# Optimization experiments

Measured on AMD Instinct MI355X. Metric: run time of the kernel, lower is better.

Reference implementation:

```python
import jax, jax.numpy as jnp
import numpy as np

D_MODEL = 128
NHEAD = 8
NLAYERS = 6
LAYER_NAMES = ['self', 'cross', 'self', 'cross', 'self', 'cross']
TEMPERATURE = 5.0
EPS = 1e-6


def _pos_encoding(x):
    # Sinusoidal 1D position encoding along the width axis. x: [N, H, W, C]
    C, W = x.shape[-1], x.shape[2]
    pos = jnp.arange(W, dtype=x.dtype)[:, None]                      # [W,1]
    div = jnp.exp(jnp.arange(0, C, 2, dtype=x.dtype) * (-np.log(10000.0) / C))
    pe = jnp.zeros((W, C), x.dtype)
    pe = pe.at[:, 0::2].set(jnp.sin(pos * div))
    pe = pe.at[:, 1::2].set(jnp.cos(pos * div))
    return x + pe[None, None]                                        # broadcast over N,H


def _linear_attention(q, k, v):
    # q,k,v: [N, H, W, nhead, dim]; kernelized linear attention along W
    Q = jax.nn.elu(q) + 1.0
    K = jax.nn.elu(k) + 1.0
    v_len = v.shape[2]
    V = v / v_len
    KV = jnp.einsum('nhsed,nhsev->nhedv', K, V)                      # [N,H,e,d,d]
    Z = 1.0 / (jnp.einsum('nhled,nhed->nhle', Q, K.sum(axis=2)) + EPS)
    return jnp.einsum('nhled,nhedv,nhle->nhlev', Q, KV, Z) * v_len


def _layer_norm(x, g, b):
    m = x.mean(-1, keepdims=True)
    v = jnp.mean((x - m) ** 2, -1, keepdims=True)
    return (x - m) / jnp.sqrt(v + 1e-5) * g + b


def _encoder_layer(x, source, Wq, Wk, Wv, Wm, W1, W2, g1, b1, g2, b2):
    x = _pos_encoding(x)
    source = _pos_encoding(source)
    bs, h, w, c = x.shape
    e, d = NHEAD, c // NHEAD
    q = (x @ Wq).reshape(bs, h, w, e, d)
    k = (source @ Wk).reshape(bs, h, w, e, d)
    v = (source @ Wv).reshape(bs, h, w, e, d)
    msg = _linear_attention(q, k, v).reshape(bs, h, w, c) @ Wm
    msg = _layer_norm(msg, g1, b1)
    msg = jnp.concatenate([x, msg], axis=-1)                         # [N,H,W,2C]
    msg = jax.nn.relu(msg @ W1) @ W2
    msg = _layer_norm(msg, g2, b2)
    return x + msg


def _forward(feat0, feat1, Wq, Wk, Wv, Wm, W1, W2, g1, b1, g2, b2):
    feat0 = feat0.transpose(0, 2, 3, 1)                              # [N,H,W,C]
    feat1 = feat1.transpose(0, 2, 3, 1)
    for i, name in enumerate(LAYER_NAMES):
        p = (Wq[i], Wk[i], Wv[i], Wm[i], W1[i], W2[i], g1[i], b1[i], g2[i], b2[i])
        if name == 'self':
            feat0 = _encoder_layer(feat0, feat0, *p)
            feat1 = _encoder_layer(feat1, feat1, *p)
        else:  # cross: sequential update (feat1 sees updated feat0), as in torch source
            feat0 = _encoder_layer(feat0, feat1, *p)
            feat1 = _encoder_layer(feat1, feat0, *p)
    w = feat0.shape[2]
    attn_mask = jnp.where(jnp.triu(jnp.ones((w, w), bool), 1), -jnp.inf, 0.0)
    attn_mask = attn_mask[None, None].astype(feat0.dtype)
    scale = feat0.shape[-1] ** 0.5
    sim = jnp.einsum('ntwc,ntlc->ntwl', feat0 / scale, feat1 / scale) / TEMPERATURE
    return sim + attn_mask


def setup_inputs() -> dict:
    key = jax.random.key(0)
    ks = jax.random.split(key, 12)
    N, C, H, W = 2, D_MODEL, 64, 640
    L, D = NLAYERS, D_MODEL
    s = 1.0 / np.sqrt(D)
    s2 = 1.0 / np.sqrt(2 * D)
    return {
        'feat0': jax.random.normal(ks[0], (N, C, H, W), jnp.float32),
        'feat1': jax.random.normal(ks[1], (N, C, H, W), jnp.float32),
        'Wq': jax.random.normal(ks[2], (L, D, D), jnp.float32) * s,
        'Wk': jax.random.normal(ks[3], (L, D, D), jnp.float32) * s,
        'Wv': jax.random.normal(ks[4], (L, D, D), jnp.float32) * s,
        'Wm': jax.random.normal(ks[5], (L, D, D), jnp.float32) * s,
        'W1': jax.random.normal(ks[6], (L, 2 * D, 2 * D), jnp.float32) * s2,
        'W2': jax.random.normal(ks[7], (L, 2 * D, D), jnp.float32) * s2,
        'g1': jnp.ones((L, D), jnp.float32),
        'b1': jnp.zeros((L, D), jnp.float32),
        'g2': jnp.ones((L, D), jnp.float32),
        'b2': jnp.zeros((L, D), jnp.float32),
    }


def reference(feat0, feat1, Wq, Wk, Wv, Wm, W1, W2, g1, b1, g2, b2):
    return _forward(feat0, feat1, Wq, Wk, Wv, Wm, W1, W2, g1, b1, g2, b2)
```

## Files before the change

### kernel.cpp

```cpp
#include <hip/hip_runtime.h>
#include <cmath>
#include <math.h>

#define TOK 81920
#define WDIM 640

typedef __attribute__((ext_vector_type(8))) short short8v;
typedef __attribute__((ext_vector_type(4))) float f32x4;

__device__ __forceinline__ short f2bf(float f) {
  union { float f; unsigned u; } x; x.f = f;
  unsigned r = (x.u + 0x7fffu + ((x.u >> 16) & 1u)) >> 16;
  return (short)r;
}
__device__ __forceinline__ float bf2f(short s) {
  union { unsigned u; float f; } x; x.u = ((unsigned)(unsigned short)s) << 16;
  return x.f;
}

__global__ __launch_bounds__(256) void pe_kernel(float* __restrict__ pe) {
  int id = blockIdx.x * 256 + threadIdx.x;
  if (id >= WDIM * 128) return;
  int w = id >> 7;
  int c = id & 127;
  float i2 = (float)(c & 126);
  float freq = expf(i2 * -0.071955784156063941f);
  float ang = (float)w * freq;
  pe[id] = (c & 1) ? cosf(ang) : sinf(ang);
}

__global__ __launch_bounds__(256) void tr_kernel(const float* __restrict__ in0,
                                                 const float* __restrict__ in1,
                                                 short* __restrict__ x0,
                                                 short* __restrict__ x1) {
  __shared__ float t[32][33];
  int w0 = blockIdx.x * 32;
  int c0 = blockIdx.y * 32;
  int z = blockIdx.z;
  int feat = z >> 7;
  int nh = z & 127;
  int n = nh >> 6, h = nh & 63;
  const float* in = feat ? in1 : in0;
  short* out = feat ? x1 : x0;
  int tx = threadIdx.x & 31, ty = threadIdx.x >> 5;
  const float* ip = in + ((n * 128 + c0) * 64 + h) * 640 + w0;
#pragma unroll
  for (int i = 0; i < 32; i += 8)
    t[ty + i][tx] = ip[(ty + i) * (64 * 640) + tx];
  __syncthreads();
  short* op = out + ((size_t)(n * 64 + h) * 640 + w0) * 128 + c0;
#pragma unroll
  for (int i = 0; i < 32; i += 8)
    op[(size_t)(ty + i) * 128 + tx] = f2bf(t[tx][ty + i]);
}

__global__ __launch_bounds__(256) void wprep_kernel(
    const float* __restrict__ Wq, const float* __restrict__ Wk,
    const float* __restrict__ Wv, const float* __restrict__ Wm,
    const float* __restrict__ W1, const float* __restrict__ W2,
    short* __restrict__ BT) {
  int id = blockIdx.x * 256 + threadIdx.x;
  if (id >= 6 * 163840) return;
  int layer = id / 163840;
  int r = id % 163840;
  float v;
  if (r < 65536) {
    int seg = r >> 14;
    int rr = r & 16383;
    int n = rr >> 7, k = rr & 127;
    const float* W = seg == 0 ? Wq : seg == 1 ? Wk : seg == 2 ? Wv : Wm;
    v = W[layer * 16384 + k * 128 + n];
  } else if (r < 131072) {
    int rr = r - 65536;
    int n = rr >> 8, k = rr & 255;
    v = W1[layer * 65536 + k * 256 + n];
  } else {
    int rr = r - 131072;
    int n = rr >> 8, k = rr & 255;
    v = W2[layer * 32768 + k * 128 + n];
  }
  BT[id] = f2bf(v);
}

__device__ __forceinline__ void load_af(const short* __restrict__ A,
                                        const float* __restrict__ pe,
                                        int bm, int wr, int l15, int lk,
                                        short8v af[4][4]) {
  const int wbase = bm % WDIM;
#pragma unroll
  for (int mf = 0; mf < 4; ++mf) {
    const int rl = wr * 64 + mf * 16 + l15;
    const short* ar = A + (size_t)(bm + rl) * 128;
    const float* pr = pe + (size_t)(wbase + rl) * 128;
#pragma unroll
    for (int ks = 0; ks < 4; ++ks) {
      const int kloc = ks * 32 + lk * 8;
      short8v xa = *(const short8v*)(ar + kloc);
      f32x4 p0 = *(const f32x4*)(pr + kloc);
      f32x4 p1 = *(const f32x4*)(pr + kloc + 4);
      short8v o;
      o[0] = f2bf(bf2f(xa[0]) + p0[0]); o[1] = f2bf(bf2f(xa[1]) + p0[1]);
      o[2] = f2bf(bf2f(xa[2]) + p0[2]); o[3] = f2bf(bf2f(xa[3]) + p0[3]);
      o[4] = f2bf(bf2f(xa[4]) + p1[0]); o[5] = f2bf(bf2f(xa[5]) + p1[1]);
      o[6] = f2bf(bf2f(xa[6]) + p1[2]); o[7] = f2bf(bf2f(xa[7]) + p1[3]);
      af[ks][mf] = o;
    }
  }
}

__device__ __forceinline__ void proj_pass(const short8v af[4][4],
                                          const short* __restrict__ WT,
                                          int bm, int wr, int wc, int l15, int lk,
                                          short* __restrict__ out) {
  f32x4 acc[4][4] = {};
#pragma unroll
  for (int ks = 0; ks < 4; ++ks) {
    const int kloc = ks * 32 + lk * 8;
    short8v bfr[4];
#pragma unroll
    for (int nf = 0; nf < 4; ++nf)
      bfr[nf] = *(const short8v*)&WT[(size_t)(wc * 64 + nf * 16 + l15) * 128 + kloc];
#pragma unroll
    for (int mf = 0; mf < 4; ++mf)
#pragma unroll
      for (int nf = 0; nf < 4; ++nf)
        acc[mf][nf] = __builtin_amdgcn_mfma_f32_16x16x32_bf16(
            af[ks][mf], bfr[nf], acc[mf][nf], 0, 0, 0);
  }
#pragma unroll
  for (int mf = 0; mf < 4; ++mf)
#pragma unroll
    for (int nf = 0; nf < 4; ++nf) {
      const int colL = wc * 64 + nf * 16 + l15;
#pragma unroll
      for (int r = 0; r < 4; ++r) {
        const int row = bm + wr * 64 + mf * 16 + lk * 4 + r;
        out[(size_t)row * 128 + colL] = f2bf(acc[mf][nf][r]);
      }
    }
}

__global__ __launch_bounds__(256) void qkv_self_kernel(
    const short* __restrict__ x0, const short* __restrict__ x1,
    const float* __restrict__ pe,
    const short* __restrict__ wqT, const short* __restrict__ wkT,
    const short* __restrict__ wvT,
    short* q0, short* k0, short* v0, short* q1, short* k1, short* v1) {
  const int tid = threadIdx.x, lane = tid & 63, wid = tid >> 6;
  const int wr = wid >> 1, wc = wid & 1;
  const int bm = blockIdx.x * 128;
  const int l15 = lane & 15, lk = lane >> 4;
  const int z = blockIdx.z;
  const short* A = z ? x1 : x0;
  short8v af[4][4];
  load_af(A, pe, bm, wr, l15, lk, af);
  proj_pass(af, wqT, bm, wr, wc, l15, lk, z ? q1 : q0);
  proj_pass(af, wkT, bm, wr, wc, l15, lk, z ? k1 : k0);
  proj_pass(af, wvT, bm, wr, wc, l15, lk, z ? v1 : v0);
}

__global__ __launch_bounds__(256) void qkv_cross_kernel(
    const short* __restrict__ xq, const short* __restrict__ xs,
    const float* __restrict__ pe,
    const short* __restrict__ wqT, const short* __restrict__ wkT,
    const short* __restrict__ wvT,
    short* qb, short* kb, short* vb) {
  const int tid = threadIdx.x, lane = tid & 63, wid = tid >> 6;
  const int wr = wid >> 1, wc = wid & 1;
  const int bm = blockIdx.x * 128;
  const int l15 = lane & 15, lk = lane >> 4;
  short8v af[4][4];
  if (blockIdx.y == 0) {
    load_af(xq, pe, bm, wr, l15, lk, af);
    proj_pass(af, wqT, bm, wr, wc, l15, lk, qb);
  } else {
    load_af(xs, pe, bm, wr, l15, lk, af);
    proj_pass(af, wkT, bm, wr, wc, l15, lk, kb);
    proj_pass(af, wvT, bm, wr, wc, l15, lk, vb);
  }
}

template <int NSC>
__global__ __launch_bounds__(256) void kv_kernel(
    const short* __restrict__ k0, const short* __restrict__ v0,
    const short* __restrict__ k1, const short* __restrict__ v1,
    float* __restrict__ kvp) {
  const int bid = blockIdx.x;
  const int sc = bid % NSC;
  const int e = bid / NSC;
  const int strip = sc / 5, chunk = sc % 5;
  const short* kb = (strip >= 128) ? k1 : k0;
  const short* vb = (strip >= 128) ? v1 : v0;
  const int nh = strip & 127;
  const size_t base = (size_t)nh * (640 * 128) + (size_t)chunk * (128 * 128) + e * 16;
  __shared__ float Ks[128][16];
  __shared__ float Vs[128][16];
  const int tid = threadIdx.x;
  const int srow = tid >> 1, shalf = (tid & 1) * 8;
  short8v k8 = *(const short8v*)&kb[base + (size_t)srow * 128 + shalf];
  short8v v8 = *(const short8v*)&vb[base + (size_t)srow * 128 + shalf];
#pragma unroll
  for (int j = 0; j < 8; ++j) {
    float kr = bf2f(k8[j]);
    Ks[srow][shalf + j] = kr > 0.f ? kr + 1.f : __expf(kr);
    Vs[srow][shalf + j] = bf2f(v8[j]);
  }
  __syncthreads();
  const int d = tid >> 4, vv = tid & 15;
  float kv = 0.f, ks = 0.f;
#pragma unroll 8
  for (int sl = 0; sl < 128; ++sl) {
    float kk = Ks[sl][d];
    kv = fmaf(kk, Vs[sl][vv], kv);
    ks += kk;
  }
  float* out = kvp + ((size_t)(strip * 8 + e) * 5 + chunk) * 272;
  out[d * 16 + vv] = kv;
  if (vv == 0) out[256 + d] = ks;
}

template <int DUAL>
__global__ __launch_bounds__(256) void apply_kernel(
    short* q0, short* q1, const float* __restrict__ kvp) {
  const int bid = blockIdx.x;
  const int strip = bid / 10, lc = bid % 10;
  __shared__ float KV8[8][16][17];
  __shared__ float KS8[8][16];
  const int tid = threadIdx.x;
  for (int idx = tid; idx < 8 * 272; idx += 256) {
    int e = idx / 272, r = idx - e * 272;
    const float* p = kvp + ((size_t)(strip * 8 + e) * 5) * 272 + r;
    float s = ((p[0] + p[272]) + (p[544] + p[816])) + p[1088];
    if (r < 256) KV8[e][r >> 4][r & 15] = s;
    else         KS8[e][r - 256] = s;
  }
  __syncthreads();
  short* qb = (DUAL && strip >= 128) ? q1 : q0;
  const int nh = strip & 127;
  const int row = lc * 64 + (tid >> 2);
  const int cb = (tid & 3) * 32;
  short* qp = qb + (size_t)nh * (640 * 128) + (size_t)row * 128 + cb;
  short8v qv0 = *(const short8v*)(qp);
  short8v qv1 = *(const short8v*)(qp + 8);
  short8v qv2 = *(const short8v*)(qp + 16);
  short8v qv3 = *(const short8v*)(qp + 24);
  float qe[32];
#pragma unroll
  for (int j = 0; j < 8; ++j) {
    float a = bf2f(qv0[j]); qe[j]      = a > 0.f ? a + 1.f : __expf(a);
    float b = bf2f(qv1[j]); qe[8 + j]  = b > 0.f ? b + 1.f : __expf(b);
    float c = bf2f(qv2[j]); qe[16 + j] = c > 0.f ? c + 1.f : __expf(c);
    float d = bf2f(qv3[j]); qe[24 + j] = d > 0.f ? d + 1.f : __expf(d);
  }
  short res[32];
#pragma unroll
  for (int h = 0; h < 2; ++h) {
    const int e = (cb >> 4) + h;
    const float* Q = qe + h * 16;
    float dz = 0.f;
#pragma unroll
    for (int dd = 0; dd < 16; ++dd) dz = fmaf(Q[dd], KS8[e][dd], dz);
    const float zi = 1.f / (dz + 1e-6f);
#pragma unroll
    for (int vv = 0; vv < 16; ++vv) {
      float o = 0.f;
#pragma unroll
      for (int dd = 0; dd < 16; ++dd) o = fmaf(Q[dd], KV8[e][dd][vv], o);
      res[h * 16 + vv] = f2bf(o * zi);
    }
  }
  short8v w0, w1, w2, w3;
#pragma unroll
  for (int j = 0; j < 8; ++j) {
    w0[j] = res[j]; w1[j] = res[8 + j]; w2[j] = res[16 + j]; w3[j] = res[24 + j];
  }
  *(short8v*)(qp)      = w0;
  *(short8v*)(qp + 8)  = w1;
  *(short8v*)(qp + 16) = w2;
  *(short8v*)(qp + 24) = w3;
}

__global__ __launch_bounds__(256) void wm_ln_kernel(
    short* oA, short* oB, const short* __restrict__ wmT,
    const float* __restrict__ g, const float* __restrict__ b) {
  const int z = blockIdx.z;
  short* o = z ? oB : oA;
  __shared__ float lds_s[2][128];
  __shared__ float lds_q[2][128];
  const int tid = threadIdx.x, lane = tid & 63, wid = tid >> 6;
  const int wr = wid >> 1, wc = wid & 1;
  const int bm = blockIdx.x * 128;
  const int l15 = lane & 15, lk = lane >> 4;
  f32x4 acc[4][4] = {};
#pragma unroll
  for (int ks = 0; ks < 4; ++ks) {
    const int kloc = ks * 32 + lk * 8;
    short8v bfr[4], afr[4];
#pragma unroll
    for (int nf = 0; nf < 4; ++nf)
      bfr[nf] = *(const short8v*)&wmT[(size_t)(wc * 64 + nf * 16 + l15) * 128 + kloc];
#pragma unroll
    for (int mf = 0; mf < 4; ++mf)
      afr[mf] = *(const short8v*)&o[(size_t)(bm + wr * 64 + mf * 16 + l15) * 128 + kloc];
#pragma unroll
    for (int mf = 0; mf < 4; ++mf)
#pragma unroll
      for (int nf = 0; nf < 4; ++nf)
        acc[mf][nf] = __builtin_amdgcn_mfma_f32_16x16x32_bf16(
            afr[mf], bfr[nf], acc[mf][nf], 0, 0, 0);
  }
#pragma unroll
  for (int mf = 0; mf < 4; ++mf)
#pragma unroll
    for (int r = 0; r < 4; ++r) {
      float s = acc[mf][0][r] + acc[mf][1][r] + acc[mf][2][r] + acc[mf][3][r];
      float qq = acc[mf][0][r] * acc[mf][0][r] + acc[mf][1][r] * acc[mf][1][r]
               + acc[mf][2][r] * acc[mf][2][r] + acc[mf][3][r] * acc[mf][3][r];
#pragma unroll
      for (int off = 1; off < 16; off <<= 1) {
        s += __shfl_xor(s, off);
        qq += __shfl_xor(qq, off);
      }
      if (l15 == 0) {
        int rl = wr * 64 + mf * 16 + lk * 4 + r;
        lds_s[wc][rl] = s;
        lds_q[wc][rl] = qq;
      }
    }
  __syncthreads();
  float gv[4], bv[4];
#pragma unroll
  for (int nf = 0; nf < 4; ++nf) {
    int c = wc * 64 + nf * 16 + l15;
    gv[nf] = g[c]; bv[nf] = b[c];
  }
#pragma unroll
  for (int mf = 0; mf < 4; ++mf)
#pragma unroll
    for (int r = 0; r < 4; ++r) {
      int rl = wr * 64 + mf * 16 + lk * 4 + r;
      float mean = (lds_s[0][rl] + lds_s[1][rl]) * (1.f / 128.f);
      float var = (lds_q[0][rl] + lds_q[1][rl]) * (1.f / 128.f) - mean * mean;
      float rstd = rsqrtf(var + 1e-5f);
#pragma unroll
      for (int nf = 0; nf < 4; ++nf) {
        float val = (acc[mf][nf][r] - mean) * rstd * gv[nf] + bv[nf];
        o[(size_t)(bm + rl) * 128 + wc * 64 + nf * 16 + l15] = f2bf(val);
      }
    }
}

__global__ __launch_bounds__(256) void w1_kernel(
    const short* __restrict__ xA, const short* __restrict__ xB,
    const short* __restrict__ mA, const short* __restrict__ mB,
    const float* __restrict__ pe, const short* __restrict__ w1T,
    short* h0A, short* h1A, short* h0B, short* h1B) {
  const int z = blockIdx.z;
  const short* x = z ? xB : xA;
  const short* m = z ? mB : mA;
  short* h0 = z ? h0B : h0A;
  short* h1 = z ? h1B : h1A;
  const int tid = threadIdx.x, lane = tid & 63, wid = tid >> 6;
  const int wr = wid >> 1, wc = wid & 1;
  const int bm = blockIdx.x * 128;
  const int l15 = lane & 15, lk = lane >> 4;
  const int wbase = bm % WDIM;
  for (int p = 0; p < 2; ++p) {
    f32x4 acc[4][4] = {};
#pragma unroll
    for (int ks = 0; ks < 8; ++ks) {
      const int kloc = ks * 32 + lk * 8;
      short8v bfr[4], afr[4];
#pragma unroll
      for (int nf = 0; nf < 4; ++nf)
        bfr[nf] = *(const short8v*)&w1T[(size_t)(p * 128 + wc * 64 + nf * 16 + l15) * 256 + kloc];
      if (ks < 4) {
#pragma unroll
        for (int mf = 0; mf < 4; ++mf) {
          const int rl = wr * 64 + mf * 16 + l15;
          short8v xa = *(const short8v*)(x + (size_t)(bm + rl) * 128 + kloc);
          const float* pr = pe + (size_t)(wbase + rl) * 128 + kloc;
          f32x4 p0 = *(const f32x4*)pr;
          f32x4 p1 = *(const f32x4*)(pr + 4);
          short8v ov;
          ov[0] = f2bf(bf2f(xa[0]) + p0[0]); ov[1] = f2bf(bf2f(xa[1]) + p0[1]);
          ov[2] = f2bf(bf2f(xa[2]) + p0[2]); ov[3] = f2bf(bf2f(xa[3]) + p0[3]);
          ov[4] = f2bf(bf2f(xa[4]) + p1[0]); ov[5] = f2bf(bf2f(xa[5]) + p1[1]);
          ov[6] = f2bf(bf2f(xa[6]) + p1[2]); ov[7] = f2bf(bf2f(xa[7]) + p1[3]);
          afr[mf] = ov;
        }
      } else {
#pragma unroll
        for (int mf = 0; mf < 4; ++mf)
          afr[mf] = *(const short8v*)&m[(size_t)(bm + wr * 64 + mf * 16 + l15) * 128 + kloc - 128];
      }
#pragma unroll
      for (int mf = 0; mf < 4; ++mf)
#pragma unroll
        for (int nf = 0; nf < 4; ++nf)
          acc[mf][nf] = __builtin_amdgcn_mfma_f32_16x16x32_bf16(
              afr[mf], bfr[nf], acc[mf][nf], 0, 0, 0);
    }
    short* h = p ? h1 : h0;
#pragma unroll
    for (int mf = 0; mf < 4; ++mf)
#pragma unroll
      for (int nf = 0; nf < 4; ++nf) {
        const int colL = wc * 64 + nf * 16 + l15;
#pragma unroll
        for (int r = 0; r < 4; ++r) {
          const int row = bm + wr * 64 + mf * 16 + lk * 4 + r;
          h[(size_t)row * 128 + colL] = f2bf(fmaxf(acc[mf][nf][r], 0.f));
        }
      }
  }
}

__global__ __launch_bounds__(256) void w2_ln_kernel(
    const short* __restrict__ h0A, const short* __restrict__ h1A,
    const short* __restrict__ h0B, const short* __restrict__ h1B,
    const short* __restrict__ w2T, short* xA, short* xB,
    const float* __restrict__ pe, const float* __restrict__ g,
    const float* __restrict__ b) {
  const int z = blockIdx.z;
  const short* h0 = z ? h0B : h0A;
  const short* h1 = z ? h1B : h1A;
  short* x = z ? xB : xA;
  __shared__ float lds_s[2][128];
  __shared__ float lds_q[2][128];
  const int tid = threadIdx.x, lane = tid & 63, wid = tid >> 6;
  const int wr = wid >> 1, wc = wid & 1;
  const int bm = blockIdx.x * 128;
  const int l15 = lane & 15, lk = lane >> 4;
  const int wbase = bm % WDIM;
  f32x4 acc[4][4] = {};
#pragma unroll
  for (int ks = 0; ks < 8; ++ks) {
    const int kloc = ks * 32 + lk * 8;
    const short* hp = (ks < 4) ? h0 : h1;
    const int kl = (ks < 4) ? kloc : kloc - 128;
    short8v bfr[4], afr[4];
#pragma unroll
    for (int nf = 0; nf < 4; ++nf)
      bfr[nf] = *(const short8v*)&w2T[(size_t)(wc * 64 + nf * 16 + l15) * 256 + kloc];
#pragma unroll
    for (int mf = 0; mf < 4; ++mf)
      afr[mf] = *(const short8v*)&hp[(size_t)(bm + wr * 64 + mf * 16 + l15) * 128 + kl];
#pragma unroll
    for (int mf = 0; mf < 4; ++mf)
#pragma unroll
      for (int nf = 0; nf < 4; ++nf)
        acc[mf][nf] = __builtin_amdgcn_mfma_f32_16x16x32_bf16(
            afr[mf], bfr[nf], acc[mf][nf], 0, 0, 0);
  }
#pragma unroll
  for (int mf = 0; mf < 4; ++mf)
#pragma unroll
    for (int r = 0; r < 4; ++r) {
      float s = acc[mf][0][r] + acc[mf][1][r] + acc[mf][2][r] + acc[mf][3][r];
      float qq = acc[mf][0][r] * acc[mf][0][r] + acc[mf][1][r] * acc[mf][1][r]
               + acc[mf][2][r] * acc[mf][2][r] + acc[mf][3][r] * acc[mf][3][r];
#pragma unroll
      for (int off = 1; off < 16; off <<= 1) {
        s += __shfl_xor(s, off);
        qq += __shfl_xor(qq, off);
      }
      if (l15 == 0) {
        int rl = wr * 64 + mf * 16 + lk * 4 + r;
        lds_s[wc][rl] = s;
        lds_q[wc][rl] = qq;
      }
    }
  __syncthreads();
  float gv[4], bv[4];
#pragma unroll
  for (int nf = 0; nf < 4; ++nf) {
    int c = wc * 64 + nf * 16 + l15;
    gv[nf] = g[c]; bv[nf] = b[c];
  }
#pragma unroll
  for (int mf = 0; mf < 4; ++mf)
#pragma unroll
    for (int r = 0; r < 4; ++r) {
      int rl = wr * 64 + mf * 16 + lk * 4 + r;
      float mean = (lds_s[0][rl] + lds_s[1][rl]) * (1.f / 128.f);
      float var = (lds_q[0][rl] + lds_q[1][rl]) * (1.f / 128.f) - mean * mean;
      float rstd = rsqrtf(var + 1e-5f);
      int row = bm + rl;
#pragma unroll
      for (int nf = 0; nf < 4; ++nf) {
        int col = wc * 64 + nf * 16 + l15;
        float ln = (acc[mf][nf][r] - mean) * rstd * gv[nf] + bv[nf];
        size_t xi = (size_t)row * 128 + col;
        float xv = bf2f(x[xi]) + pe[(size_t)(wbase + rl) * 128 + col] + ln;
        x[xi] = f2bf(xv);
      }
    }
}

__global__ __launch_bounds__(256) void sim_mfma(const short* __restrict__ f0,
                                                const short* __restrict__ f1,
                                                float* __restrict__ out) {
  const int fid = (blockIdx.z * 5 + blockIdx.y) * 5 + blockIdx.x;
  const int c8 = fid & 7, kk_ = fid >> 3;
  const int nt = c8 * 16 + kk_ / 25;
  const int r2 = kk_ % 25;
  const int bw = (r2 % 5) * 128;
  const int bl = (r2 / 5) * 128;
  const int tid = threadIdx.x;
  const int lane = tid & 63;
  const int wid = tid >> 6;
  const int wr = wid >> 1, wc = wid & 1;
  const short* __restrict__ A = f0 + (size_t)nt * 640 * 128;
  const short* __restrict__ B = f1 + (size_t)nt * 640 * 128;
  const int l15 = lane & 15;
  const int lk = lane >> 4;
  f32x4 acc[4][4] = {};
#pragma unroll
  for (int ks = 0; ks < 4; ++ks) {
    const int kloc = ks * 32 + lk * 8;
    short8v afr[4], bfr[4];
#pragma unroll
    for (int mf = 0; mf < 4; ++mf)
      afr[mf] = *(const short8v*)&A[(size_t)(bw + wr * 64 + mf * 16 + l15) * 128 + kloc];
#pragma unroll
    for (int nf = 0; nf < 4; ++nf)
      bfr[nf] = *(const short8v*)&B[(size_t)(bl + wc * 64 + nf * 16 + l15) * 128 + kloc];
#pragma unroll
    for (int mf = 0; mf < 4; ++mf)
#pragma unroll
      for (int nf = 0; nf < 4; ++nf)
        acc[mf][nf] = __builtin_amdgcn_mfma_f32_16x16x32_bf16(
            afr[mf], bfr[nf], acc[mf][nf], 0, 0, 0);
  }
#pragma unroll
  for (int mf = 0; mf < 4; ++mf)
#pragma unroll
    for (int nf = 0; nf < 4; ++nf) {
      const int l = bl + wc * 64 + nf * 16 + l15;
#pragma unroll
      for (int r = 0; r < 4; ++r) {
        const int w = bw + wr * 64 + mf * 16 + lk * 4 + r;
        float v = acc[mf][nf][r] * (1.f / 640.f);
        if (l > w) v = -1e30f;
        out[((size_t)nt * 640 + w) * 640 + l] = v;
      }
    }
}

extern "C" void kernel_launch(void* const* d_in, const int* in_sizes, int n_in,
                              void* d_out, int out_size, void* d_ws, size_t ws_size,
                              hipStream_t stream) {
  (void)in_sizes; (void)n_in; (void)out_size; (void)ws_size;
  const float* feat0 = (const float*)d_in[0];
  const float* feat1 = (const float*)d_in[1];
  const float* Wq = (const float*)d_in[2];
  const float* Wk = (const float*)d_in[3];
  const float* Wv = (const float*)d_in[4];
  const float* Wm = (const float*)d_in[5];
  const float* W1 = (const float*)d_in[6];
  const float* W2 = (const float*)d_in[7];
  const float* g1 = (const float*)d_in[8];
  const float* b1 = (const float*)d_in[9];
  const float* g2 = (const float*)d_in[10];
  const float* b2 = (const float*)d_in[11];

  float* wsf = (float*)d_ws;
  const size_t U = (size_t)TOK * 128;
  float* pe = wsf;
  short* x0 = (short*)(wsf + 81920);
  short* x1 = x0 + U;
  short* q0 = x1 + U;
  short* k0 = q0 + U;
  short* v0 = k0 + U;
  short* q1 = v0 + U;
  short* k1 = q1 + U;
  short* v1 = k1 + U;
  short* bt = v1 + U;
  float* kvp = (float*)(bt + 983040);

  dim3 blk(256);
  pe_kernel<<<dim3(320), blk, 0, stream>>>(pe);
  tr_kernel<<<dim3(20, 4, 256), blk, 0, stream>>>(feat0, feat1, x0, x1);
  wprep_kernel<<<dim3((6 * 163840 + 255) / 256), blk, 0, stream>>>(
      Wq, Wk, Wv, Wm, W1, W2, bt);

  const int NB = TOK / 128;
  for (int i = 0; i < 6; ++i) {
    const short* bt_i = bt + (size_t)i * 163840;
    const short* wqT = bt_i;
    const short* wkT = bt_i + 16384;
    const short* wvT = bt_i + 32768;
    const short* wmT = bt_i + 49152;
    const short* w1T = bt_i + 65536;
    const short* w2T = bt_i + 131072;
    const float* g1_i = g1 + i * 128;
    const float* b1_i = b1 + i * 128;
    const float* g2_i = g2 + i * 128;
    const float* b2_i = b2 + i * 128;
    if ((i & 1) == 0) {
      qkv_self_kernel<<<dim3(NB, 1, 2), blk, 0, stream>>>(
          x0, x1, pe, wqT, wkT, wvT, q0, k0, v0, q1, k1, v1);
      kv_kernel<1280><<<dim3(8 * 1280), blk, 0, stream>>>(k0, v0, k1, v1, kvp);
      apply_kernel<1><<<dim3(2560), blk, 0, stream>>>(q0, q1, kvp);
      wm_ln_kernel<<<dim3(NB, 1, 2), blk, 0, stream>>>(q0, q1, wmT, g1_i, b1_i);
      w1_kernel<<<dim3(NB, 1, 2), blk, 0, stream>>>(
          x0, x1, q0, q1, pe, w1T, k0, v0, k1, v1);
      w2_ln_kernel<<<dim3(NB, 1, 2), blk, 0, stream>>>(
          k0, v0, k1, v1, w2T, x0, x1, pe, g2_i, b2_i);
    } else {
      qkv_cross_kernel<<<dim3(NB, 2), blk, 0, stream>>>(
          x0, x1, pe, wqT, wkT, wvT, q0, k0, v0);
      kv_kernel<640><<<dim3(8 * 640), blk, 0, stream>>>(k0, v0, k0, v0, kvp);
      apply_kernel<0><<<dim3(1280), blk, 0, stream>>>(q0, q0, kvp);
      wm_ln_kernel<<<dim3(NB, 1, 1), blk, 0, stream>>>(q0, q0, wmT, g1_i, b1_i);
      w1_kernel<<<dim3(NB, 1, 1), blk, 0, stream>>>(
          x0, x0, q0, q0, pe, w1T, k0, v0, k0, v0);
      w2_ln_kernel<<<dim3(NB, 1, 1), blk, 0, stream>>>(
          k0, v0, k0, v0, w2T, x0, x0, pe, g2_i, b2_i);

      qkv_cross_kernel<<<dim3(NB, 2), blk, 0, stream>>>(
          x1, x0, pe, wqT, wkT, wvT, q0, k0, v0);
      kv_kernel<640><<<dim3(8 * 640), blk, 0, stream>>>(k0, v0, k0, v0, kvp);
      apply_kernel<0><<<dim3(1280), blk, 0, stream>>>(q0, q0, kvp);
      wm_ln_kernel<<<dim3(NB, 1, 1), blk, 0, stream>>>(q0, q0, wmT, g1_i, b1_i);
      w1_kernel<<<dim3(NB, 1, 1), blk, 0, stream>>>(
          x1, x1, q0, q0, pe, w1T, k0, v0, k0, v0);
      w2_ln_kernel<<<dim3(NB, 1, 1), blk, 0, stream>>>(
          k0, v0, k0, v0, w2T, x1, x1, pe, g2_i, b2_i);
    }
  }
  sim_mfma<<<dim3(5, 5, 128), blk, 0, stream>>>(x0, x1, (float*)d_out);
}
```

Measured before the change: 2.846 ms.

## Fuse attention apply with Wm+LayerNorm, and W1/W2 into one FFN kernel

The attention-apply kernel now keeps its output tile in shared memory and immediately multiplies it by Wm with MFMA and applies LayerNorm, replacing the separate wm_ln kernel. The W1 and W2 GEMMs are merged into a single 512-thread ffn_kernel over 64-row tiles, with the ReLU hidden activations staged in LDS. This removes the global round-trips of the attention message and the 256-wide hidden tensor, plus two kernel launches per pass. The cost is more LDS per block, and smaller tiles that reload weights more often.

```diff
diff --git a/kernel.cpp b/kernel.cpp
--- a/kernel.cpp
+++ b/kernel.cpp
@@ -220,12 +220,15 @@
 }
 
 template <int DUAL>
-__global__ __launch_bounds__(256) void apply_kernel(
-    short* q0, short* q1, const float* __restrict__ kvp) {
+__global__ __launch_bounds__(256) void apply_wm_kernel(
+    short* q0, short* q1, const float* __restrict__ kvp,
+    const short* __restrict__ wmT,
+    const float* __restrict__ g, const float* __restrict__ b) {
   const int bid = blockIdx.x;
   const int strip = bid / 10, lc = bid % 10;
   __shared__ float KV8[8][16][17];
   __shared__ float KS8[8][16];
+  __shared__ short oS[64][136];
   const int tid = threadIdx.x;
   for (int idx = tid; idx < 8 * 272; idx += 256) {
     int e = idx / 272, r = idx - e * 272;
@@ -237,7 +240,8 @@
   __syncthreads();
   short* qb = (DUAL && strip >= 128) ? q1 : q0;
   const int nh = strip & 127;
-  const int row = lc * 64 + (tid >> 2);
+  const int lrow = tid >> 2;
+  const int row = lc * 64 + lrow;
   const int cb = (tid & 3) * 32;
   short* qp = qb + (size_t)nh * (640 * 128) + (size_t)row * 128 + cb;
   short8v qv0 = *(const short8v*)(qp);
@@ -248,9 +252,9 @@
 #pragma unroll
   for (int j = 0; j < 8; ++j) {
     float a = bf2f(qv0[j]); qe[j]      = a > 0.f ? a + 1.f : __expf(a);
-    float b = bf2f(qv1[j]); qe[8 + j]  = b > 0.f ? b + 1.f : __expf(b);
-    float c = bf2f(qv2[j]); qe[16 + j] = c > 0.f ? c + 1.f : __expf(c);
-    float d = bf2f(qv3[j]); qe[24 + j] = d > 0.f ? d + 1.f : __expf(d);
+    float c1 = bf2f(qv1[j]); qe[8 + j]  = c1 > 0.f ? c1 + 1.f : __expf(c1);
+    float c2 = bf2f(qv2[j]); qe[16 + j] = c2 > 0.f ? c2 + 1.f : __expf(c2);
+    float c3 = bf2f(qv3[j]); qe[24 + j] = c3 > 0.f ? c3 + 1.f : __expf(c3);
   }
   short res[32];
 #pragma unroll
@@ -274,110 +278,83 @@
   for (int j = 0; j < 8; ++j) {
     w0[j] = res[j]; w1[j] = res[8 + j]; w2[j] = res[16 + j]; w3[j] = res[24 + j];
   }
-  *(short8v*)(qp)      = w0;
-  *(short8v*)(qp + 8)  = w1;
-  *(short8v*)(qp + 16) = w2;
-  *(short8v*)(qp + 24) = w3;
-}
-
-__global__ __launch_bounds__(256) void wm_ln_kernel(
-    short* oA, short* oB, const short* __restrict__ wmT,
+  *(short8v*)&oS[lrow][cb]      = w0;
+  *(short8v*)&oS[lrow][cb + 8]  = w1;
+  *(short8v*)&oS[lrow][cb + 16] = w2;
+  *(short8v*)&oS[lrow][cb + 24] = w3;
+  __syncthreads();
+  const int lane = tid & 63, w = tid >> 6;
+  const int l15 = lane & 15, lk = lane >> 4;
+  f32x4 acc[8] = {};
+#pragma unroll
+  for (int ks = 0; ks < 4; ++ks) {
+    const int kloc = ks * 32 + lk * 8;
+    short8v afr = *(const short8v*)&oS[w * 16 + l15][kloc];
+    short8v bfr[8];
+#pragma unroll
+    for (int nf = 0; nf < 8; ++nf)
+      bfr[nf] = *(const short8v*)&wmT[(size_t)(nf * 16 + l15) * 128 + kloc];
+#pragma unroll
+    for (int nf = 0; nf < 8; ++nf)
+      acc[nf] = __builtin_amdgcn_mfma_f32_16x16x32_bf16(afr, bfr[nf], acc[nf], 0, 0, 0);
+  }
+  float gv[8], bv[8];
+#pragma unroll
+  for (int nf = 0; nf < 8; ++nf) { gv[nf] = g[nf * 16 + l15]; bv[nf] = b[nf * 16 + l15]; }
+#pragma unroll
+  for (int r = 0; r < 4; ++r) {
+    float s = 0.f, qq = 0.f;
+#pragma unroll
+    for (int nf = 0; nf < 8; ++nf) {
+      s += acc[nf][r];
+      qq = fmaf(acc[nf][r], acc[nf][r], qq);
+    }
+#pragma unroll
+    for (int off = 1; off < 16; off <<= 1) {
+      s += __shfl_xor(s, off);
+      qq += __shfl_xor(qq, off);
+    }
+    float mean = s * (1.f / 128.f);
+    float var = qq * (1.f / 128.f) - mean * mean;
+    float rstd = rsqrtf(var + 1e-5f);
+    const int grow = lc * 64 + w * 16 + lk * 4 + r;
+    short* mp = qb + (size_t)nh * (640 * 128) + (size_t)grow * 128;
+#pragma unroll
+    for (int nf = 0; nf < 8; ++nf)
+      mp[nf * 16 + l15] = f2bf((acc[nf][r] - mean) * rstd * gv[nf] + bv[nf]);
+  }
+}
+
+__global__ __launch_bounds__(512, 4) void ffn_kernel(
+    short* xA, short* xB,
+    const short* __restrict__ mA, const short* __restrict__ mB,
+    const float* __restrict__ pe, const short* __restrict__ w1T,
+    const short* __restrict__ w2T,
     const float* __restrict__ g, const float* __restrict__ b) {
   const int z = blockIdx.z;
-  short* o = z ? oB : oA;
-  __shared__ float lds_s[2][128];
-  __shared__ float lds_q[2][128];
-  const int tid = threadIdx.x, lane = tid & 63, wid = tid >> 6;
-  const int wr = wid >> 1, wc = wid & 1;
-  const int bm = blockIdx.x * 128;
-  const int l15 = lane & 15, lk = lane >> 4;
-  f32x4 acc[4][4] = {};
-#pragma unroll
-  for (int ks = 0; ks < 4; ++ks) {
-    const int kloc = ks * 32 + lk * 8;
-    short8v bfr[4], afr[4];
-#pragma unroll
-    for (int nf = 0; nf < 4; ++nf)
-      bfr[nf] = *(const short8v*)&wmT[(size_t)(wc * 64 + nf * 16 + l15) * 128 + kloc];
-#pragma unroll
-    for (int mf = 0; mf < 4; ++mf)
-      afr[mf] = *(const short8v*)&o[(size_t)(bm + wr * 64 + mf * 16 + l15) * 128 + kloc];
-#pragma unroll
-    for (int mf = 0; mf < 4; ++mf)
-#pragma unroll
-      for (int nf = 0; nf < 4; ++nf)
-        acc[mf][nf] = __builtin_amdgcn_mfma_f32_16x16x32_bf16(
-            afr[mf], bfr[nf], acc[mf][nf], 0, 0, 0);
-  }
-#pragma unroll
-  for (int mf = 0; mf < 4; ++mf)
-#pragma unroll
-    for (int r = 0; r < 4; ++r) {
-      float s = acc[mf][0][r] + acc[mf][1][r] + acc[mf][2][r] + acc[mf][3][r];
-      float qq = acc[mf][0][r] * acc[mf][0][r] + acc[mf][1][r] * acc[mf][1][r]
-               + acc[mf][2][r] * acc[mf][2][r] + acc[mf][3][r] * acc[mf][3][r];
-#pragma unroll
-      for (int off = 1; off < 16; off <<= 1) {
-        s += __shfl_xor(s, off);
-        qq += __shfl_xor(qq, off);
-      }
-      if (l15 == 0) {
-        int rl = wr * 64 + mf * 16 + lk * 4 + r;
-        lds_s[wc][rl] = s;
-        lds_q[wc][rl] = qq;
-      }
-    }
-  __syncthreads();
-  float gv[4], bv[4];
-#pragma unroll
-  for (int nf = 0; nf < 4; ++nf) {
-    int c = wc * 64 + nf * 16 + l15;
-    gv[nf] = g[c]; bv[nf] = b[c];
-  }
-#pragma unroll
-  for (int mf = 0; mf < 4; ++mf)
-#pragma unroll
-    for (int r = 0; r < 4; ++r) {
-      int rl = wr * 64 + mf * 16 + lk * 4 + r;
-      float mean = (lds_s[0][rl] + lds_s[1][rl]) * (1.f / 128.f);
-      float var = (lds_q[0][rl] + lds_q[1][rl]) * (1.f / 128.f) - mean * mean;
-      float rstd = rsqrtf(var + 1e-5f);
-#pragma unroll
-      for (int nf = 0; nf < 4; ++nf) {
-        float val = (acc[mf][nf][r] - mean) * rstd * gv[nf] + bv[nf];
-        o[(size_t)(bm + rl) * 128 + wc * 64 + nf * 16 + l15] = f2bf(val);
-      }
-    }
-}
-
-__global__ __launch_bounds__(256) void w1_kernel(
-    const short* __restrict__ xA, const short* __restrict__ xB,
-    const short* __restrict__ mA, const short* __restrict__ mB,
-    const float* __restrict__ pe, const short* __restrict__ w1T,
-    short* h0A, short* h1A, short* h0B, short* h1B) {
-  const int z = blockIdx.z;
-  const short* x = z ? xB : xA;
+  short* x = z ? xB : xA;
   const short* m = z ? mB : mA;
-  short* h0 = z ? h0B : h0A;
-  short* h1 = z ? h1B : h1A;
-  const int tid = threadIdx.x, lane = tid & 63, wid = tid >> 6;
-  const int wr = wid >> 1, wc = wid & 1;
-  const int bm = blockIdx.x * 128;
+  __shared__ short hS[64][264];
+  __shared__ float lds_s[4][64];
+  __shared__ float lds_q[4][64];
+  const int tid = threadIdx.x, lane = tid & 63, w = tid >> 6;
+  const int wrh = w & 1, wch = w >> 1;
+  const int bm = blockIdx.x * 64;
   const int l15 = lane & 15, lk = lane >> 4;
   const int wbase = bm % WDIM;
-  for (int p = 0; p < 2; ++p) {
-    f32x4 acc[4][4] = {};
+  {
+    f32x4 acc[2][4] = {};
 #pragma unroll
     for (int ks = 0; ks < 8; ++ks) {
       const int kloc = ks * 32 + lk * 8;
-      short8v bfr[4], afr[4];
+      short8v bfr[4], afr[2];
 #pragma unroll
       for (int nf = 0; nf < 4; ++nf)
-        bfr[nf] = *(const short8v*)&w1T[(size_t)(p * 128 + wc * 64 + nf * 16 + l15) * 256 + kloc];
-      if (ks < 4) {
-#pragma unroll
-        for (int mf = 0; mf < 4; ++mf) {
-          const int rl = wr * 64 + mf * 16 + l15;
+        bfr[nf] = *(const short8v*)&w1T[(size_t)(wch * 64 + nf * 16 + l15) * 256 + kloc];
+#pragma unroll
+      for (int mf = 0; mf < 2; ++mf) {
+        const int rl = wrh * 32 + mf * 16 + l15;
+        if (ks < 4) {
           short8v xa = *(const short8v*)(x + (size_t)(bm + rl) * 128 + kloc);
           const float* pr = pe + (size_t)(wbase + rl) * 128 + kloc;
           f32x4 p0 = *(const f32x4*)pr;
@@ -388,109 +365,85 @@
           ov[4] = f2bf(bf2f(xa[4]) + p1[0]); ov[5] = f2bf(bf2f(xa[5]) + p1[1]);
           ov[6] = f2bf(bf2f(xa[6]) + p1[2]); ov[7] = f2bf(bf2f(xa[7]) + p1[3]);
           afr[mf] = ov;
+        } else {
+          afr[mf] = *(const short8v*)(m + (size_t)(bm + rl) * 128 + kloc - 128);
         }
-      } else {
-#pragma unroll
-        for (int mf = 0; mf < 4; ++mf)
-          afr[mf] = *(const short8v*)&m[(size_t)(bm + wr * 64 + mf * 16 + l15) * 128 + kloc - 128];
-      }
-#pragma unroll
-      for (int mf = 0; mf < 4; ++mf)
+      }
+#pragma unroll
+      for (int mf = 0; mf < 2; ++mf)
 #pragma unroll
         for (int nf = 0; nf < 4; ++nf)
           acc[mf][nf] = __builtin_amdgcn_mfma_f32_16x16x32_bf16(
               afr[mf], bfr[nf], acc[mf][nf], 0, 0, 0);
     }
-    short* h = p ? h1 : h0;
-#pragma unroll
-    for (int mf = 0; mf < 4; ++mf)
+#pragma unroll
+    for (int mf = 0; mf < 2; ++mf)
 #pragma unroll
       for (int nf = 0; nf < 4; ++nf) {
-        const int colL = wc * 64 + nf * 16 + l15;
-#pragma unroll
-        for (int r = 0; r < 4; ++r) {
-          const int row = bm + wr * 64 + mf * 16 + lk * 4 + r;
-          h[(size_t)row * 128 + colL] = f2bf(fmaxf(acc[mf][nf][r], 0.f));
-        }
-      }
-  }
-}
-
-__global__ __launch_bounds__(256) void w2_ln_kernel(
-    const short* __restrict__ h0A, const short* __restrict__ h1A,
-    const short* __restrict__ h0B, const short* __restrict__ h1B,
-    const short* __restrict__ w2T, short* xA, short* xB,
-    const float* __restrict__ pe, const float* __restrict__ g,
-    const float* __restrict__ b) {
-  const int z = blockIdx.z;
-  const short* h0 = z ? h0B : h0A;
-  const short* h1 = z ? h1B : h1A;
-  short* x = z ? xB : xA;
-  __shared__ float lds_s[2][128];
-  __shared__ float lds_q[2][128];
-  const int tid = threadIdx.x, lane = tid & 63, wid = tid >> 6;
-  const int wr = wid >> 1, wc = wid & 1;
-  const int bm = blockIdx.x * 128;
-  const int l15 = lane & 15, lk = lane >> 4;
-  const int wbase = bm % WDIM;
-  f32x4 acc[4][4] = {};
+        const int col = wch * 64 + nf * 16 + l15;
+#pragma unroll
+        for (int r = 0; r < 4; ++r)
+          hS[wrh * 32 + mf * 16 + lk * 4 + r][col] = f2bf(fmaxf(acc[mf][nf][r], 0.f));
+      }
+  }
+  __syncthreads();
+  f32x4 acc2[2][2] = {};
 #pragma unroll
   for (int ks = 0; ks < 8; ++ks) {
     const int kloc = ks * 32 + lk * 8;
-    const short* hp = (ks < 4) ? h0 : h1;
-    const int kl = (ks < 4) ? kloc : kloc - 128;
-    short8v bfr[4], afr[4];
-#pragma unroll
-    for (int nf = 0; nf < 4; ++nf)
-      bfr[nf] = *(const short8v*)&w2T[(size_t)(wc * 64 + nf * 16 + l15) * 256 + kloc];
-#pragma unroll
-    for (int mf = 0; mf < 4; ++mf)
-      afr[mf] = *(const short8v*)&hp[(size_t)(bm + wr * 64 + mf * 16 + l15) * 128 + kl];
-#pragma unroll
-    for (int mf = 0; mf < 4; ++mf)
-#pragma unroll
-      for (int nf = 0; nf < 4; ++nf)
-        acc[mf][nf] = __builtin_amdgcn_mfma_f32_16x16x32_bf16(
-            afr[mf], bfr[nf], acc[mf][nf], 0, 0, 0);
-  }
-#pragma unroll
-  for (int mf = 0; mf < 4; ++mf)
+    short8v bfr[2], afr[2];
+#pragma unroll
+    for (int nf = 0; nf < 2; ++nf)
+      bfr[nf] = *(const short8v*)&w2T[(size_t)(wch * 32 + nf * 16 + l15) * 256 + kloc];
+#pragma unroll
+    for (int mf = 0; mf < 2; ++mf)
+      afr[mf] = *(const short8v*)&hS[wrh * 32 + mf * 16 + l15][kloc];
+#pragma unroll
+    for (int mf = 0; mf < 2; ++mf)
+#pragma unroll
+      for (int nf = 0; nf < 2; ++nf)
+        acc2[mf][nf] = __builtin_amdgcn_mfma_f32_16x16x32_bf16(
+            afr[mf], bfr[nf], acc2[mf][nf], 0, 0, 0);
+  }
+#pragma unroll
+  for (int mf = 0; mf < 2; ++mf)
 #pragma unroll
     for (int r = 0; r < 4; ++r) {
-      float s = acc[mf][0][r] + acc[mf][1][r] + acc[mf][2][r] + acc[mf][3][r];
-      float qq = acc[mf][0][r] * acc[mf][0][r] + acc[mf][1][r] * acc[mf][1][r]
-               + acc[mf][2][r] * acc[mf][2][r] + acc[mf][3][r] * acc[mf][3][r];
+      float s = acc2[mf][0][r] + acc2[mf][1][r];
+      float qq = acc2[mf][0][r] * acc2[mf][0][r] + acc2[mf][1][r] * acc2[mf][1][r];
 #pragma unroll
       for (int off = 1; off < 16; off <<= 1) {
         s += __shfl_xor(s, off);
         qq += __shfl_xor(qq, off);
       }
       if (l15 == 0) {
-        int rl = wr * 64 + mf * 16 + lk * 4 + r;
-        lds_s[wc][rl] = s;
-        lds_q[wc][rl] = qq;
+        int rl = wrh * 32 + mf * 16 + lk * 4 + r;
+        lds_s[wch][rl] = s;
+        lds_q[wch][rl] = qq;
       }
     }
   __syncthreads();
-  float gv[4], bv[4];
-#pragma unroll
-  for (int nf = 0; nf < 4; ++nf) {
-    int c = wc * 64 + nf * 16 + l15;
+  float gv[2], bv[2];
+#pragma unroll
+  for (int nf = 0; nf < 2; ++nf) {
+    int c = wch * 32 + nf * 16 + l15;
     gv[nf] = g[c]; bv[nf] = b[c];
   }
 #pragma unroll
-  for (int mf = 0; mf < 4; ++mf)
+  for (int mf = 0; mf < 2; ++mf)
 #pragma unroll
     for (int r = 0; r < 4; ++r) {
-      int rl = wr * 64 + mf * 16 + lk * 4 + r;
-      float mean = (lds_s[0][rl] + lds_s[1][rl]) * (1.f / 128.f);
-      float var = (lds_q[0][rl] + lds_q[1][rl]) * (1.f / 128.f) - mean * mean;
+      int rl = wrh * 32 + mf * 16 + lk * 4 + r;
+      float ssum = (lds_s[0][rl] + lds_s[1][rl]) + (lds_s[2][rl] + lds_s[3][rl]);
+      float qsum = (lds_q[0][rl] + lds_q[1][rl]) + (lds_q[2][rl] + lds_q[3][rl]);
+      float mean = ssum * (1.f / 128.f);
+      float var = qsum * (1.f / 128.f) - mean * mean;
       float rstd = rsqrtf(var + 1e-5f);
       int row = bm + rl;
 #pragma unroll
-      for (int nf = 0; nf < 4; ++nf) {
-        int col = wc * 64 + nf * 16 + l15;
-        float ln = (acc[mf][nf][r] - mean) * rstd * gv[nf] + bv[nf];
+      for (int nf = 0; nf < 2; ++nf) {
+        int col = wch * 32 + nf * 16 + l15;
+        float ln = (acc2[mf][nf][r] - mean) * rstd * gv[nf] + bv[nf];
         size_t xi = (size_t)row * 128 + col;
         float xv = bf2f(x[xi]) + pe[(size_t)(wbase + rl) * 128 + col] + ln;
         x[xi] = f2bf(xv);
@@ -586,6 +539,7 @@
       Wq, Wk, Wv, Wm, W1, W2, bt);
 
   const int NB = TOK / 128;
+  const int NB2 = TOK / 64;
   for (int i = 0; i < 6; ++i) {
     const short* bt_i = bt + (size_t)i * 163840;
     const short* wqT = bt_i;
@@ -602,32 +556,23 @@
       qkv_self_kernel<<<dim3(NB, 1, 2), blk, 0, stream>>>(
           x0, x1, pe, wqT, wkT, wvT, q0, k0, v0, q1, k1, v1);
       kv_kernel<1280><<<dim3(8 * 1280), blk, 0, stream>>>(k0, v0, k1, v1, kvp);
-      apply_kernel<1><<<dim3(2560), blk, 0, stream>>>(q0, q1, kvp);
-      wm_ln_kernel<<<dim3(NB, 1, 2), blk, 0, stream>>>(q0, q1, wmT, g1_i, b1_i);
-      w1_kernel<<<dim3(NB, 1, 2), blk, 0, stream>>>(
-          x0, x1, q0, q1, pe, w1T, k0, v0, k1, v1);
-      w2_ln_kernel<<<dim3(NB, 1, 2), blk, 0, stream>>>(
-          k0, v0, k1, v1, w2T, x0, x1, pe, g2_i, b2_i);
+      apply_wm_kernel<1><<<dim3(2560), blk, 0, stream>>>(q0, q1, kvp, wmT, g1_i, b1_i);
+      ffn_kernel<<<dim3(NB2, 1, 2), dim3(512), 0, stream>>>(
+          x0, x1, q0, q1, pe, w1T, w2T, g2_i, b2_i);
     } else {
       qkv_cross_kernel<<<dim3(NB, 2), blk, 0, stream>>>(
           x0, x1, pe, wqT, wkT, wvT, q0, k0, v0);
       kv_kernel<640><<<dim3(8 * 640), blk, 0, stream>>>(k0, v0, k0, v0, kvp);
-      apply_kernel<0><<<dim3(1280), blk, 0, stream>>>(q0, q0, kvp);
-      wm_ln_kernel<<<dim3(NB, 1, 1), blk, 0, stream>>>(q0, q0, wmT, g1_i, b1_i);
-      w1_kernel<<<dim3(NB, 1, 1), blk, 0, stream>>>(
-          x0, x0, q0, q0, pe, w1T, k0, v0, k0, v0);
-      w2_ln_kernel<<<dim3(NB, 1, 1), blk, 0, stream>>>(
-          k0, v0, k0, v0, w2T, x0, x0, pe, g2_i, b2_i);
+      apply_wm_kernel<0><<<dim3(1280), blk, 0, stream>>>(q0, q0, kvp, wmT, g1_i, b1_i);
+      ffn_kernel<<<dim3(NB2, 1, 1), dim3(512), 0, stream>>>(
+          x0, x0, q0, q0, pe, w1T, w2T, g2_i, b2_i);
 
       qkv_cross_kernel<<<dim3(NB, 2), blk, 0, stream>>>(
           x1, x0, pe, wqT, wkT, wvT, q0, k0, v0);
       kv_kernel<640><<<dim3(8 * 640), blk, 0, stream>>>(k0, v0, k0, v0, kvp);
-      apply_kernel<0><<<dim3(1280), blk, 0, stream>>>(q0, q0, kvp);
-      wm_ln_kernel<<<dim3(NB, 1, 1), blk, 0, stream>>>(q0, q0, wmT, g1_i, b1_i);
-      w1_kernel<<<dim3(NB, 1, 1), blk, 0, stream>>>(
-          x1, x1, q0, q0, pe, w1T, k0, v0, k0, v0);
-      w2_ln_kernel<<<dim3(NB, 1, 1), blk, 0, stream>>>(
-          k0, v0, k0, v0, w2T, x1, x1, pe, g2_i, b2_i);
+      apply_wm_kernel<0><<<dim3(1280), blk, 0, stream>>>(q0, q0, kvp, wmT, g1_i, b1_i);
+      ffn_kernel<<<dim3(NB2, 1, 1), dim3(512), 0, stream>>>(
+          x1, x1, q0, q0, pe, w1T, w2T, g2_i, b2_i);
     }
   }
   sim_mfma<<<dim3(5, 5, 128), blk, 0, stream>>>(x0, x1, (float*)d_out);
```

Result: faster. 2.740 ms (-3.8%).

## Fuse linear-attention apply with Wm projection and LayerNorm via LDS staging

Applied to the files above, without the earlier changes.

Merges the attention apply kernel and the Wm GEMM plus LayerNorm kernel into one. Each block stages its 64 attention-output rows as bf16 in shared memory and runs the 128x128 Wm matmul with MFMA from there. LayerNorm is then computed per row with in-wave shuffles only. This removes one kernel launch per attention stage and a global write and re-read of the message tensor. The cost is extra LDS per block and a new 64-row tile shape, where each wave loads the full Wm B-fragments.

```diff
diff --git a/kernel.cpp b/kernel.cpp
--- a/kernel.cpp
+++ b/kernel.cpp
@@ -220,12 +220,15 @@
 }
 
 template <int DUAL>
-__global__ __launch_bounds__(256) void apply_kernel(
-    short* q0, short* q1, const float* __restrict__ kvp) {
+__global__ __launch_bounds__(256) void apply_wm_kernel(
+    short* q0, short* q1, const float* __restrict__ kvp,
+    const short* __restrict__ wmT,
+    const float* __restrict__ g, const float* __restrict__ b) {
   const int bid = blockIdx.x;
   const int strip = bid / 10, lc = bid % 10;
   __shared__ float KV8[8][16][17];
   __shared__ float KS8[8][16];
+  __shared__ short oS[64][136];
   const int tid = threadIdx.x;
   for (int idx = tid; idx < 8 * 272; idx += 256) {
     int e = idx / 272, r = idx - e * 272;
@@ -237,7 +240,8 @@
   __syncthreads();
   short* qb = (DUAL && strip >= 128) ? q1 : q0;
   const int nh = strip & 127;
-  const int row = lc * 64 + (tid >> 2);
+  const int lrow = tid >> 2;
+  const int row = lc * 64 + lrow;
   const int cb = (tid & 3) * 32;
   short* qp = qb + (size_t)nh * (640 * 128) + (size_t)row * 128 + cb;
   short8v qv0 = *(const short8v*)(qp);
@@ -248,9 +252,9 @@
 #pragma unroll
   for (int j = 0; j < 8; ++j) {
     float a = bf2f(qv0[j]); qe[j]      = a > 0.f ? a + 1.f : __expf(a);
-    float b = bf2f(qv1[j]); qe[8 + j]  = b > 0.f ? b + 1.f : __expf(b);
-    float c = bf2f(qv2[j]); qe[16 + j] = c > 0.f ? c + 1.f : __expf(c);
-    float d = bf2f(qv3[j]); qe[24 + j] = d > 0.f ? d + 1.f : __expf(d);
+    float c1 = bf2f(qv1[j]); qe[8 + j]  = c1 > 0.f ? c1 + 1.f : __expf(c1);
+    float c2 = bf2f(qv2[j]); qe[16 + j] = c2 > 0.f ? c2 + 1.f : __expf(c2);
+    float c3 = bf2f(qv3[j]); qe[24 + j] = c3 > 0.f ? c3 + 1.f : __expf(c3);
   }
   short res[32];
 #pragma unroll
@@ -274,80 +278,51 @@
   for (int j = 0; j < 8; ++j) {
     w0[j] = res[j]; w1[j] = res[8 + j]; w2[j] = res[16 + j]; w3[j] = res[24 + j];
   }
-  *(short8v*)(qp)      = w0;
-  *(short8v*)(qp + 8)  = w1;
-  *(short8v*)(qp + 16) = w2;
-  *(short8v*)(qp + 24) = w3;
-}
-
-__global__ __launch_bounds__(256) void wm_ln_kernel(
-    short* oA, short* oB, const short* __restrict__ wmT,
-    const float* __restrict__ g, const float* __restrict__ b) {
-  const int z = blockIdx.z;
-  short* o = z ? oB : oA;
-  __shared__ float lds_s[2][128];
-  __shared__ float lds_q[2][128];
-  const int tid = threadIdx.x, lane = tid & 63, wid = tid >> 6;
-  const int wr = wid >> 1, wc = wid & 1;
-  const int bm = blockIdx.x * 128;
+  *(short8v*)&oS[lrow][cb]      = w0;
+  *(short8v*)&oS[lrow][cb + 8]  = w1;
+  *(short8v*)&oS[lrow][cb + 16] = w2;
+  *(short8v*)&oS[lrow][cb + 24] = w3;
+  __syncthreads();
+  const int lane = tid & 63, w = tid >> 6;
   const int l15 = lane & 15, lk = lane >> 4;
-  f32x4 acc[4][4] = {};
+  f32x4 acc[8] = {};
 #pragma unroll
   for (int ks = 0; ks < 4; ++ks) {
     const int kloc = ks * 32 + lk * 8;
-    short8v bfr[4], afr[4];
-#pragma unroll
-    for (int nf = 0; nf < 4; ++nf)
-      bfr[nf] = *(const short8v*)&wmT[(size_t)(wc * 64 + nf * 16 + l15) * 128 + kloc];
-#pragma unroll
-    for (int mf = 0; mf < 4; ++mf)
-      afr[mf] = *(const short8v*)&o[(size_t)(bm + wr * 64 + mf * 16 + l15) * 128 + kloc];
-#pragma unroll
-    for (int mf = 0; mf < 4; ++mf)
-#pragma unroll
-      for (int nf = 0; nf < 4; ++nf)
-        acc[mf][nf] = __builtin_amdgcn_mfma_f32_16x16x32_bf16(
-            afr[mf], bfr[nf], acc[mf][nf], 0, 0, 0);
-  }
-#pragma unroll
-  for (int mf = 0; mf < 4; ++mf)
-#pragma unroll
-    for (int r = 0; r < 4; ++r) {
-      float s = acc[mf][0][r] + acc[mf][1][r] + acc[mf][2][r] + acc[mf][3][r];
-      float qq = acc[mf][0][r] * acc[mf][0][r] + acc[mf][1][r] * acc[mf][1][r]
-               + acc[mf][2][r] * acc[mf][2][r] + acc[mf][3][r] * acc[mf][3][r];
-#pragma unroll
-      for (int off = 1; off < 16; off <<= 1) {
-        s += __shfl_xor(s, off);
-        qq += __shfl_xor(qq, off);
-      }
-      if (l15 == 0) {
-        int rl = wr * 64 + mf * 16 + lk * 4 + r;
-        lds_s[wc][rl] = s;
-        lds_q[wc][rl] = qq;
-      }
-    }
-  __syncthreads();
-  float gv[4], bv[4];
-#pragma unroll
-  for (int nf = 0; nf < 4; ++nf) {
-    int c = wc * 64 + nf * 16 + l15;
-    gv[nf] = g[c]; bv[nf] = b[c];
-  }
-#pragma unroll
-  for (int mf = 0; mf < 4; ++mf)
-#pragma unroll
-    for (int r = 0; r < 4; ++r) {
-      int rl = wr * 64 + mf * 16 + lk * 4 + r;
-      float mean = (lds_s[0][rl] + lds_s[1][rl]) * (1.f / 128.f);
-      float var = (lds_q[0][rl] + lds_q[1][rl]) * (1.f / 128.f) - mean * mean;
-      float rstd = rsqrtf(var + 1e-5f);
-#pragma unroll
-      for (int nf = 0; nf < 4; ++nf) {
-        float val = (acc[mf][nf][r] - mean) * rstd * gv[nf] + bv[nf];
-        o[(size_t)(bm + rl) * 128 + wc * 64 + nf * 16 + l15] = f2bf(val);
-      }
-    }
+    short8v afr = *(const short8v*)&oS[w * 16 + l15][kloc];
+    short8v bfr[8];
+#pragma unroll
+    for (int nf = 0; nf < 8; ++nf)
+      bfr[nf] = *(const short8v*)&wmT[(size_t)(nf * 16 + l15) * 128 + kloc];
+#pragma unroll
+    for (int nf = 0; nf < 8; ++nf)
+      acc[nf] = __builtin_amdgcn_mfma_f32_16x16x32_bf16(afr, bfr[nf], acc[nf], 0, 0, 0);
+  }
+  float gv[8], bv[8];
+#pragma unroll
+  for (int nf = 0; nf < 8; ++nf) { gv[nf] = g[nf * 16 + l15]; bv[nf] = b[nf * 16 + l15]; }
+#pragma unroll
+  for (int r = 0; r < 4; ++r) {
+    float s = 0.f, qq = 0.f;
+#pragma unroll
+    for (int nf = 0; nf < 8; ++nf) {
+      s += acc[nf][r];
+      qq = fmaf(acc[nf][r], acc[nf][r], qq);
+    }
+#pragma unroll
+    for (int off = 1; off < 16; off <<= 1) {
+      s += __shfl_xor(s, off);
+      qq += __shfl_xor(qq, off);
+    }
+    float mean = s * (1.f / 128.f);
+    float var = qq * (1.f / 128.f) - mean * mean;
+    float rstd = rsqrtf(var + 1e-5f);
+    const int grow = lc * 64 + w * 16 + lk * 4 + r;
+    short* mp = qb + (size_t)nh * (640 * 128) + (size_t)grow * 128;
+#pragma unroll
+    for (int nf = 0; nf < 8; ++nf)
+      mp[nf * 16 + l15] = f2bf((acc[nf][r] - mean) * rstd * gv[nf] + bv[nf]);
+  }
 }
 
 __global__ __launch_bounds__(256) void w1_kernel(
@@ -602,8 +577,7 @@
       qkv_self_kernel<<<dim3(NB, 1, 2), blk, 0, stream>>>(
           x0, x1, pe, wqT, wkT, wvT, q0, k0, v0, q1, k1, v1);
       kv_kernel<1280><<<dim3(8 * 1280), blk, 0, stream>>>(k0, v0, k1, v1, kvp);
-      apply_kernel<1><<<dim3(2560), blk, 0, stream>>>(q0, q1, kvp);
-      wm_ln_kernel<<<dim3(NB, 1, 2), blk, 0, stream>>>(q0, q1, wmT, g1_i, b1_i);
+      apply_wm_kernel<1><<<dim3(2560), blk, 0, stream>>>(q0, q1, kvp, wmT, g1_i, b1_i);
       w1_kernel<<<dim3(NB, 1, 2), blk, 0, stream>>>(
           x0, x1, q0, q1, pe, w1T, k0, v0, k1, v1);
       w2_ln_kernel<<<dim3(NB, 1, 2), blk, 0, stream>>>(
@@ -612,8 +586,7 @@
       qkv_cross_kernel<<<dim3(NB, 2), blk, 0, stream>>>(
           x0, x1, pe, wqT, wkT, wvT, q0, k0, v0);
       kv_kernel<640><<<dim3(8 * 640), blk, 0, stream>>>(k0, v0, k0, v0, kvp);
-      apply_kernel<0><<<dim3(1280), blk, 0, stream>>>(q0, q0, kvp);
-      wm_ln_kernel<<<dim3(NB, 1, 1), blk, 0, stream>>>(q0, q0, wmT, g1_i, b1_i);
+      apply_wm_kernel<0><<<dim3(1280), blk, 0, stream>>>(q0, q0, kvp, wmT, g1_i, b1_i);
       w1_kernel<<<dim3(NB, 1, 1), blk, 0, stream>>>(
           x0, x0, q0, q0, pe, w1T, k0, v0, k0, v0);
       w2_ln_kernel<<<dim3(NB, 1, 1), blk, 0, stream>>>(
@@ -622,8 +595,7 @@
       qkv_cross_kernel<<<dim3(NB, 2), blk, 0, stream>>>(
           x1, x0, pe, wqT, wkT, wvT, q0, k0, v0);
       kv_kernel<640><<<dim3(8 * 640), blk, 0, stream>>>(k0, v0, k0, v0, kvp);
-      apply_kernel<0><<<dim3(1280), blk, 0, stream>>>(q0, q0, kvp);
-      wm_ln_kernel<<<dim3(NB, 1, 1), blk, 0, stream>>>(q0, q0, wmT, g1_i, b1_i);
+      apply_wm_kernel<0><<<dim3(1280), blk, 0, stream>>>(q0, q0, kvp, wmT, g1_i, b1_i);
       w1_kernel<<<dim3(NB, 1, 1), blk, 0, stream>>>(
           x1, x1, q0, q0, pe, w1T, k0, v0, k0, v0);
       w2_ln_kernel<<<dim3(NB, 1, 1), blk, 0, stream>>>(
```

Result: faster. 2.767 ms (-2.8%).
